# Performance work log

Measured on AMD Instinct MI355X. Metric: run time of the kernel, lower is better.

Reference implementation:

```python
import jax, jax.numpy as jnp
import numpy as np

EPS_NORM = 1e-5   # RMSLayerNorm eps (hardcoded in __init__)
Q_EPS = 1e-5      # clamp floor for quantization scales (BitMat convention)


def _rmsnorm(x, w, eps):
    var = jnp.mean(jnp.square(x), axis=-1, keepdims=True)
    return x * jax.lax.rsqrt(var + eps) * w


def _weight_quant(w):
    # ternary (1.58-bit) quantization: scale = 1/mean(|W|), round+clip to {-1,0,1}
    scale = 1.0 / jnp.maximum(jnp.mean(jnp.abs(w)), Q_EPS)
    wq = jnp.clip(jnp.round(w * scale), -1.0, 1.0)
    return wq, scale


def _act_quant(x):
    # per-token int8 quantization: scale = 127/max(|x|) along last dim
    scale = 127.0 / jnp.maximum(jnp.max(jnp.abs(x), axis=-1, keepdims=True), Q_EPS)
    xq = jnp.clip(jnp.round(x * scale), -128.0, 127.0)
    return xq, scale


def setup_inputs() -> dict:
    key = jax.random.key(0)
    k1, k2 = jax.random.split(key)
    B, S, D = 4, 4096, 4096  # in_features == out_features == 4096
    x = jax.random.normal(k1, (B, S, D), dtype=jnp.float32)
    norm_weight = jnp.ones((D,), dtype=jnp.float32)
    # kaiming_normal fan_out relu: std = sqrt(2/out_features)
    weight = jax.random.normal(k2, (D, D), dtype=jnp.float32) * np.sqrt(2.0 / D)
    return {"x": x, "norm_weight": norm_weight, "weight": weight}


def reference(x, norm_weight, weight):
    h = _rmsnorm(x, norm_weight, EPS_NORM)            # [B,S,D]
    wq, sw = _weight_quant(weight)                    # [O,D], scalar
    hq, sx = _act_quant(h)                            # [B,S,D], [B,S,1]
    # integer-valued GEMM then dequant by both scales
    y = jnp.einsum('bsd,od->bso', hq, wq) / (sx * sw)
    return y
```

## Files before the change

### kernel.cpp

```cpp
#include <hip/hip_runtime.h>
#include <cstdint>
#include <cstddef>

typedef int v4i  __attribute__((ext_vector_type(4)));
typedef int v16i __attribute__((ext_vector_type(16)));

__device__ __forceinline__ void load_lds16(const void* g, void* l) {
    __builtin_amdgcn_global_load_lds(
        (const __attribute__((address_space(1))) void*)g,
        (__attribute__((address_space(3))) void*)l,
        16, 0, 0);
}

__global__ void wabs_sum_kernel(const float4* __restrict__ w4,
                                double* __restrict__ acc, int n4) {
    double s = 0.0;
    for (int i = blockIdx.x * blockDim.x + threadIdx.x; i < n4;
         i += gridDim.x * blockDim.x) {
        float4 v = w4[i];
        s += (double)fabsf(v.x) + (double)fabsf(v.y) +
             (double)fabsf(v.z) + (double)fabsf(v.w);
    }
    for (int o = 32; o > 0; o >>= 1) s += __shfl_down(s, o);
    __shared__ double sb[4];
    const int wid = threadIdx.x >> 6, lane = threadIdx.x & 63;
    if (lane == 0) sb[wid] = s;
    __syncthreads();
    if (threadIdx.x == 0) atomicAdd(acc, sb[0] + sb[1] + sb[2] + sb[3]);
}

__device__ __forceinline__ float sw_from_sum(const double* sump, int n) {
    float mean = (float)(*sump / (double)n);
    return 1.0f / fmaxf(mean, 1e-5f);
}

__global__ void wquant_kernel(const float4* __restrict__ w4,
                              const double* __restrict__ sump,
                              char4* __restrict__ wq4, int n4, int n) {
    const float s = sw_from_sum(sump, n);
    int i = blockIdx.x * blockDim.x + threadIdx.x;
    if (i >= n4) return;
    float4 v = w4[i];
    char4 q;
    q.x = (signed char)(int)fmaxf(-1.f, fminf(1.f, rintf(v.x * s)));
    q.y = (signed char)(int)fmaxf(-1.f, fminf(1.f, rintf(v.y * s)));
    q.z = (signed char)(int)fmaxf(-1.f, fminf(1.f, rintf(v.z * s)));
    q.w = (signed char)(int)fmaxf(-1.f, fminf(1.f, rintf(v.w * s)));
    wq4[i] = q;
}

__global__ __launch_bounds__(256) void act_quant_kernel(
    const float* __restrict__ x, const float* __restrict__ nw,
    const double* __restrict__ sump, int wcount,
    signed char* __restrict__ hq, float* __restrict__ rscale, int D) {
    const int m = blockIdx.x;
    const int t = threadIdx.x;
    const float4* xr  = (const float4*)(x + (size_t)m * D);
    const float4* nw4 = (const float4*)nw;

    float4 v[4];
    float ss = 0.f;
#pragma unroll
    for (int i = 0; i < 4; ++i) {
        v[i] = xr[t + 256 * i];
        ss += v[i].x * v[i].x + v[i].y * v[i].y +
              v[i].z * v[i].z + v[i].w * v[i].w;
    }
    for (int o = 32; o > 0; o >>= 1) ss += __shfl_down(ss, o);
    __shared__ float sb[4];
    const int wid = t >> 6, lane = t & 63;
    if (lane == 0) sb[wid] = ss;
    __syncthreads();
    const float var  = (sb[0] + sb[1] + sb[2] + sb[3]) / (float)D;
    const float rstd = (float)(1.0 / sqrt((double)var + 1e-5));
    __syncthreads();

    float mx = 0.f;
#pragma unroll
    for (int i = 0; i < 4; ++i) {
        float4 g = nw4[t + 256 * i];
        v[i].x = v[i].x * rstd * g.x;
        v[i].y = v[i].y * rstd * g.y;
        v[i].z = v[i].z * rstd * g.z;
        v[i].w = v[i].w * rstd * g.w;
        mx = fmaxf(mx, fmaxf(fmaxf(fabsf(v[i].x), fabsf(v[i].y)),
                             fmaxf(fabsf(v[i].z), fabsf(v[i].w))));
    }
    for (int o = 32; o > 0; o >>= 1) mx = fmaxf(mx, __shfl_down(mx, o));
    if (lane == 0) sb[wid] = mx;
    __syncthreads();
    const float mxa   = fmaxf(fmaxf(sb[0], sb[1]), fmaxf(sb[2], sb[3]));
    const float scale = 127.0f / fmaxf(mxa, 1e-5f);

    char4* hq4 = (char4*)(hq + (size_t)m * D);
#pragma unroll
    for (int i = 0; i < 4; ++i) {
        char4 q;
        q.x = (signed char)(int)fmaxf(-128.f, fminf(127.f, rintf(v[i].x * scale)));
        q.y = (signed char)(int)fmaxf(-128.f, fminf(127.f, rintf(v[i].y * scale)));
        q.z = (signed char)(int)fmaxf(-128.f, fminf(127.f, rintf(v[i].z * scale)));
        q.w = (signed char)(int)fmaxf(-128.f, fminf(127.f, rintf(v[i].w * scale)));
        hq4[t + 256 * i] = q;
    }
    if (t == 0) {
        const float sw = sw_from_sum(sump, wcount);
        rscale[m] = 1.0f / (scale * sw);
    }
}

constexpr int BM = 256, BN = 256, BK = 64;

template<bool DO_STAGE, int VM>
__device__ __forceinline__ void gemm_tile(
    int t, signed char (*As)[BM * BK], signed char (*Bs)[BN * BK],
    const signed char* aSrc, const signed char* bSrc, int K, int ldsOff,
    int wm, int wn, int r32, int h, v16i (&acc)[4][2])
{
    const int buf = t & 3;
    const int rb  = r32 & 3;
#pragma unroll
    for (int ks = 0; ks < 2; ++ks) {
        v4i af[4], bf[2];
        const int slot = ((2 * ks + h) ^ rb) * 16;
#pragma unroll
        for (int mf = 0; mf < 4; ++mf)
            af[mf] = *(const v4i*)&As[buf][(wm * 128 + mf * 32 + r32) * BK + slot];
#pragma unroll
        for (int nf = 0; nf < 2; ++nf)
            bf[nf] = *(const v4i*)&Bs[buf][(wn * 64 + nf * 32 + r32) * BK + slot];

        if (DO_STAGE) {
            const size_t kt = (size_t)(t + 3) * BK;
            if (ks == 0) {
                signed char* d = &As[(t + 3) & 3][ldsOff];
                load_lds16(aSrc + kt, d);
                load_lds16(aSrc + kt + (size_t)16 * K, d + 1024);
            } else {
                signed char* d = &Bs[(t + 3) & 3][ldsOff];
                load_lds16(bSrc + kt, d);
                load_lds16(bSrc + kt + (size_t)16 * K, d + 1024);
            }
        }
        __builtin_amdgcn_s_barrier();
        __builtin_amdgcn_s_setprio(1);
#pragma unroll
        for (int mf = 0; mf < 4; ++mf)
#pragma unroll
            for (int nf = 0; nf < 2; ++nf)
                acc[mf][nf] = __builtin_amdgcn_mfma_i32_32x32x32_i8(
                    af[mf], bf[nf], acc[mf][nf], 0, 0, 0);
        __builtin_amdgcn_s_setprio(0);
        if (ks == 1) {
            if (VM == 8)      asm volatile("s_waitcnt vmcnt(8)" ::: "memory");
            else if (VM == 4) asm volatile("s_waitcnt vmcnt(4)" ::: "memory");
            else if (VM == 0) asm volatile("s_waitcnt vmcnt(0)" ::: "memory");
        }
        __builtin_amdgcn_s_barrier();
    }
}

__global__ __launch_bounds__(512, 2) void gemm_i8_kernel(
    const signed char* __restrict__ A, const signed char* __restrict__ B,
    const float* __restrict__ rscale, float* __restrict__ out,
    int M, int N, int K) {
    __shared__ signed char As[4][BM * BK];
    __shared__ signed char Bs[4][BN * BK];

    const int tid  = threadIdx.x;
    const int wave = tid >> 6;
    const int lane = tid & 63;
    const int wm   = wave >> 2;
    const int wn   = wave & 3;
    const int r32  = lane & 31;
    const int h    = lane >> 5;

    const int nwg = gridDim.x * gridDim.y;
    int lin = blockIdx.y * gridDim.x + blockIdx.x;
    lin = (lin & 7) * (nwg >> 3) + (lin >> 3);
    const int m0 = (lin / (int)gridDim.x) * BM;
    const int n0 = (lin % (int)gridDim.x) * BN;

    const int lrow = lane >> 2;
    const int lswz = ((lane & 3) ^ (lrow & 3)) * 16;
    const signed char* aSrc = A + (size_t)(m0 + wave * 32 + lrow) * K + lswz;
    const signed char* bSrc = B + (size_t)(n0 + wave * 32 + lrow) * K + lswz;
    const int ldsOff = wave * 2048;

    v16i acc[4][2] = {};

#pragma unroll
    for (int p = 0; p < 3; ++p) {
        const size_t kt = (size_t)p * BK;
        signed char* da = &As[p][ldsOff];
        signed char* db = &Bs[p][ldsOff];
        load_lds16(aSrc + kt, da);
        load_lds16(aSrc + kt + (size_t)16 * K, da + 1024);
        load_lds16(bSrc + kt, db);
        load_lds16(bSrc + kt + (size_t)16 * K, db + 1024);
    }
    asm volatile("s_waitcnt vmcnt(8)" ::: "memory");
    __builtin_amdgcn_s_barrier();

    const int NT = K >> 6;
    int t = 0;
    for (; t < NT - 3; ++t)
        gemm_tile<true, 8>(t, As, Bs, aSrc, bSrc, K, ldsOff, wm, wn, r32, h, acc);
    gemm_tile<false, 4>(NT - 3, As, Bs, aSrc, bSrc, K, ldsOff, wm, wn, r32, h, acc);
    gemm_tile<false, 0>(NT - 2, As, Bs, aSrc, bSrc, K, ldsOff, wm, wn, r32, h, acc);
    gemm_tile<false, -1>(NT - 1, As, Bs, aSrc, bSrc, K, ldsOff, wm, wn, r32, h, acc);

#pragma unroll
    for (int mf = 0; mf < 4; ++mf) {
#pragma unroll
        for (int reg = 0; reg < 16; ++reg) {
            const int m = m0 + wm * 128 + mf * 32 + (reg & 3) + 8 * (reg >> 2) + 4 * h;
            const float rs = rscale[m];
            const size_t rowoff = (size_t)m * N + n0 + wn * 64 + r32;
#pragma unroll
            for (int nf = 0; nf < 2; ++nf)
                out[rowoff + nf * 32] = (float)acc[mf][nf][reg] * rs;
        }
    }
}

extern "C" void kernel_launch(void* const* d_in, const int* in_sizes, int n_in,
                              void* d_out, int out_size, void* d_ws, size_t ws_size,
                              hipStream_t stream) {
    const float* x  = (const float*)d_in[0];
    const float* nw = (const float*)d_in[1];
    const float* w  = (const float*)d_in[2];
    const int D = in_sizes[1];
    const int M = in_sizes[0] / D;
    const int O = in_sizes[2] / D;
    const int WN = O * D;

    char* ws = (char*)d_ws;
    double* d_sum    = (double*)(ws + 0);
    float*  d_rscale = (float*)(ws + 128);
    size_t off = 128 + (size_t)M * sizeof(float);
    off = (off + 255) & ~(size_t)255;
    signed char* d_wq = (signed char*)(ws + off);
    off += (size_t)WN;
    off = (off + 255) & ~(size_t)255;
    signed char* d_hq = (signed char*)(ws + off);

    hipMemsetAsync(d_sum, 0, sizeof(double), stream);

    wabs_sum_kernel<<<4096, 256, 0, stream>>>((const float4*)w, d_sum, WN / 4);

    wquant_kernel<<<(WN / 4 + 255) / 256, 256, 0, stream>>>(
        (const float4*)w, d_sum, (char4*)d_wq, WN / 4, WN);

    act_quant_kernel<<<M, 256, 0, stream>>>(x, nw, d_sum, WN, d_hq, d_rscale, D);

    dim3 grid(O / 256, M / 256);
    gemm_i8_kernel<<<grid, 512, 0, stream>>>(d_hq, d_wq, d_rscale,
                                             (float*)d_out, M, O, D);
}
```

Measured before the change: 833.9 us.

## Issue all tile loads up front, drop mid-tile barrier, change LDS swizzle

Each K-tile now issues all four global-to-LDS prefetch loads at its start, reads both k-substeps of A/B fragments into registers, then runs all 16 MFMAs followed by a single wait and barrier. This halves the barriers per tile and gives the loads more time to overlap with compute. The LDS XOR swizzle now keys on row bits 2-3 instead of bits 0-1, with matching changes on the write and read sides, to reduce bank conflicts. Holding both substeps of fragments raises register pressure under the 2-workgroup launch bounds.

```diff
diff --git a/kernel.cpp b/kernel.cpp
--- a/kernel.cpp
+++ b/kernel.cpp
@@ -110,53 +110,52 @@
 
 constexpr int BM = 256, BN = 256, BK = 64;
 
-template<bool DO_STAGE, int VM>
+template<bool STAGE, int VM>
 __device__ __forceinline__ void gemm_tile(
     int t, signed char (*As)[BM * BK], signed char (*Bs)[BN * BK],
     const signed char* aSrc, const signed char* bSrc, int K, int ldsOff,
     int wm, int wn, int r32, int h, v16i (&acc)[4][2])
 {
     const int buf = t & 3;
-    const int rb  = r32 & 3;
+
+    if (STAGE) {
+        const size_t kt = (size_t)(t + 3) * BK;
+        signed char* da = &As[(t + 3) & 3][ldsOff];
+        signed char* db = &Bs[(t + 3) & 3][ldsOff];
+        load_lds16(aSrc + kt, da);
+        load_lds16(aSrc + kt + (size_t)16 * K, da + 1024);
+        load_lds16(bSrc + kt, db);
+        load_lds16(bSrc + kt + (size_t)16 * K, db + 1024);
+    }
+
+    const int rs = (r32 >> 2) & 3;
+    v4i af[2][4], bf[2][2];
 #pragma unroll
     for (int ks = 0; ks < 2; ++ks) {
-        v4i af[4], bf[2];
-        const int slot = ((2 * ks + h) ^ rb) * 16;
+        const int slot = ((2 * ks + h) ^ rs) * 16;
 #pragma unroll
         for (int mf = 0; mf < 4; ++mf)
-            af[mf] = *(const v4i*)&As[buf][(wm * 128 + mf * 32 + r32) * BK + slot];
+            af[ks][mf] = *(const v4i*)&As[buf][(wm * 128 + mf * 32 + r32) * BK + slot];
 #pragma unroll
         for (int nf = 0; nf < 2; ++nf)
-            bf[nf] = *(const v4i*)&Bs[buf][(wn * 64 + nf * 32 + r32) * BK + slot];
-
-        if (DO_STAGE) {
-            const size_t kt = (size_t)(t + 3) * BK;
-            if (ks == 0) {
-                signed char* d = &As[(t + 3) & 3][ldsOff];
-                load_lds16(aSrc + kt, d);
-                load_lds16(aSrc + kt + (size_t)16 * K, d + 1024);
-            } else {
-                signed char* d = &Bs[(t + 3) & 3][ldsOff];
-                load_lds16(bSrc + kt, d);
-                load_lds16(bSrc + kt + (size_t)16 * K, d + 1024);
-            }
-        }
-        __builtin_amdgcn_s_barrier();
-        __builtin_amdgcn_s_setprio(1);
+            bf[ks][nf] = *(const v4i*)&Bs[buf][(wn * 64 + nf * 32 + r32) * BK + slot];
+    }
+
+    __builtin_amdgcn_s_setprio(1);
+#pragma unroll
+    for (int ks = 0; ks < 2; ++ks)
 #pragma unroll
         for (int mf = 0; mf < 4; ++mf)
 #pragma unroll
             for (int nf = 0; nf < 2; ++nf)
                 acc[mf][nf] = __builtin_amdgcn_mfma_i32_32x32x32_i8(
-                    af[mf], bf[nf], acc[mf][nf], 0, 0, 0);
-        __builtin_amdgcn_s_setprio(0);
-        if (ks == 1) {
-            if (VM == 8)      asm volatile("s_waitcnt vmcnt(8)" ::: "memory");
-            else if (VM == 4) asm volatile("s_waitcnt vmcnt(4)" ::: "memory");
-            else if (VM == 0) asm volatile("s_waitcnt vmcnt(0)" ::: "memory");
-        }
-        __builtin_amdgcn_s_barrier();
-    }
+                    af[ks][mf], bf[ks][nf], acc[mf][nf], 0, 0, 0);
+    __builtin_amdgcn_s_setprio(0);
+
+    if (VM == 8)      asm volatile("s_waitcnt vmcnt(8)" ::: "memory");
+    else if (VM == 4) asm volatile("s_waitcnt vmcnt(4)" ::: "memory");
+    else if (VM == 0) asm volatile("s_waitcnt vmcnt(0)" ::: "memory");
+    __builtin_amdgcn_s_barrier();
 }
 
 __global__ __launch_bounds__(512, 2) void gemm_i8_kernel(
@@ -181,7 +180,7 @@
     const int n0 = (lin % (int)gridDim.x) * BN;
 
     const int lrow = lane >> 2;
-    const int lswz = ((lane & 3) ^ (lrow & 3)) * 16;
+    const int lswz = ((lane & 3) ^ ((lane >> 4) & 3)) * 16;
     const signed char* aSrc = A + (size_t)(m0 + wave * 32 + lrow) * K + lswz;
     const signed char* bSrc = B + (size_t)(n0 + wave * 32 + lrow) * K + lswz;
     const int ldsOff = wave * 2048;
```

New measurement: 860.6 us. +3.2%, slower.
